# Optimization experiments

Measured on AMD Instinct MI355X. Metric: run time of the kernel, lower is better.

## Reference

```python
import math
import jax, jax.numpy as jnp
import numpy as np

C1, D, NUM_HEADS, K_CH = 150, 32, 4, 10
GLOBAL_TOPK_RATIO = 0.08


def _pos2d(h, w, dim):
    d2 = dim // 2
    div = jnp.exp(jnp.arange(0, d2, 2, dtype=jnp.float32) * (-(math.log(10000.0) / d2)))
    def axis_pe(n):
        ang = jnp.arange(n, dtype=jnp.float32)[:, None] * div[None, :]
        pe = jnp.zeros((n, d2), dtype=jnp.float32)
        pe = pe.at[:, 0::2].set(jnp.sin(ang))
        pe = pe.at[:, 1::2].set(jnp.cos(ang))
        return pe
    pe_y = axis_pe(h)  # [h, d2]
    pe_x = axis_pe(w)  # [w, d2]
    return jnp.concatenate([
        jnp.broadcast_to(pe_y[:, None, :], (h, w, d2)),
        jnp.broadcast_to(pe_x[None, :, :], (h, w, d2)),
    ], axis=-1)  # [h, w, dim]


def setup_inputs() -> dict:
    key = jax.random.key(0)
    ks = jax.random.split(key, 7)
    B = 1024
    return {
        "x": jax.random.uniform(ks[0], (B, 1, 28, 28), dtype=jnp.float32),
        "conv1_w": jax.random.normal(ks[1], (C1, 1, 9, 9), dtype=jnp.float32) * 0.05,
        "channel_embed": jax.random.normal(ks[2], (C1, D), dtype=jnp.float32) * 0.02,
        "in_proj_w": jax.random.normal(ks[3], (3 * D, D), dtype=jnp.float32) * (1.0 / math.sqrt(D)),
        "in_proj_b": jnp.zeros((3 * D,), dtype=jnp.float32),
        "out_proj_w": jax.random.normal(ks[4], (D, D), dtype=jnp.float32) * (1.0 / math.sqrt(D)),
        "out_proj_b": jnp.zeros((D,), dtype=jnp.float32),
    }


def reference(x, conv1_w, channel_embed, in_proj_w, in_proj_b, out_proj_w, out_proj_b):
    # conv1 + relu: [B,1,28,28] -> [B,150,14,14]
    A = jax.nn.relu(jax.lax.conv_general_dilated(
        x, conv1_w, window_strides=(2, 2), padding=((4, 4), (4, 4)),
        dimension_numbers=("NCHW", "OIHW", "NCHW")))
    B, C, H, W = A.shape
    total = C * H * W
    k_global = max(1, int(math.ceil(GLOBAL_TOPK_RATIO * total)))
    A_flat = A.reshape(B, -1)
    # global kthvalue threshold: k_global-th largest per sample
    thresh = jax.lax.top_k(A_flat, k_global)[0][:, -1:]
    A_global = (A_flat * (A_flat >= thresh)).reshape(B, C, H, W)
    # per-location channel top-k + scatter
    v = jnp.transpose(A_global, (0, 2, 3, 1))  # [B,H,W,C]
    topv, topi = jax.lax.top_k(v, K_CH)        # [B,H,W,k]
    N = B * H * W
    logits = jnp.zeros((N, C), v.dtype).at[
        jnp.arange(N)[:, None], topi.reshape(N, K_CH)
    ].set(topv.reshape(N, K_CH)).reshape(v.shape)
    # normalize by per-sample global max (guard zero)
    flat_logits = logits.reshape(B, -1)
    gmax = jnp.max(flat_logits, axis=1, keepdims=True)
    normed = jnp.where(gmax == 0, 0.0, flat_logits / jnp.where(gmax == 0, 1.0, gmax))
    sparse_weights = normed.reshape(logits.shape)  # [B,H,W,C]
    # channel embedding + 2D sinusoidal PE
    loc_emb = jnp.einsum("bhwc,cd->bhwd", sparse_weights, channel_embed)
    loc_emb = loc_emb + _pos2d(H, W, D)[None]
    seq = loc_emb.reshape(B, H * W, D)
    # 1-layer MHA (self-attention, batch_first)
    qkv = seq @ in_proj_w.T + in_proj_b  # [B,S,3D]
    q, k, vv = jnp.split(qkv, 3, axis=-1)
    hd = D // NUM_HEADS
    def heads(t):
        return jnp.transpose(t.reshape(B, H * W, NUM_HEADS, hd), (0, 2, 1, 3))
    q, k, vv = heads(q), heads(k), heads(vv)
    attn = jax.nn.softmax(jnp.einsum("bnsd,bntd->bnst", q, k) / math.sqrt(hd), axis=-1)
    ctx = jnp.einsum("bnst,bntd->bnsd", attn, vv)
    ctx = jnp.transpose(ctx, (0, 2, 1, 3)).reshape(B, H * W, D)
    attn_out = ctx @ out_proj_w.T + out_proj_b  # [B, 196, 32]
    return attn_out
```

## Files before the change

kernel.cpp:

```cpp
#include <hip/hip_runtime.h>
#include <math.h>

#define NC1 150
#define HW 196
#define NB 1024
#define DD 32
#define NHD 4
#define HDIM 8
#define KG 2352
#define KCH 10
#define CAP 48
#define CVS 49
#define CES 36

#define UNI_F 17552
#define XT_OFF 0
#define WT_OFF 8232
#define CV_OFF 0
#define CC_OFF 9604
#define CNT_OFF 11956
#define CE_OFF 12152

__global__ void pos2d_kernel(float* __restrict__ pos) {
  int i = blockIdx.x * 256 + threadIdx.x;
  if (i >= HW * DD) return;
  int s = i >> 5, d = i & 31;
  int h = s / 14, w = s % 14;
  int p = (d < 16) ? h : w;
  int dd = (d < 16) ? d : d - 16;
  int j = dd >> 1;
  float dv = expf(-(logf(10000.0f) / 16.0f) * (float)(2 * j));
  float ang = (float)p * dv;
  pos[i] = (dd & 1) ? cosf(ang) : sinf(ang);
}

__global__ void prep_kernel(const float* __restrict__ cw, float* __restrict__ wtg) {
  int i = blockIdx.x * 256 + threadIdx.x;
  if (i >= 84 * 152) return;
  int k = i / 152, c = i - k * 152;
  wtg[i] = (k < 81 && c < NC1) ? cw[c * 81 + k] : 0.f;
}

__global__ __launch_bounds__(1024, 8) void fused_kernel(const float* __restrict__ x,
                                                        const float* __restrict__ wtg,
                                                        const float* __restrict__ CE,
                                                        const float* __restrict__ pos,
                                                        float* __restrict__ seqo) {
  __shared__ alignas(16) float uni[UNI_F];
  __shared__ alignas(16) float xs[784];
  __shared__ unsigned hist[2048];
  __shared__ unsigned wsum[4];
  __shared__ unsigned s_prefix, s_krem, s_max;

  int b = blockIdx.x, tid = threadIdx.x;
  int lane = tid & 63, wid = tid >> 6;

  if (tid < 196) ((float4*)xs)[tid] = ((const float4*)(x + (size_t)b * 784))[tid];
  if (tid == 0) { s_prefix = 0u; s_krem = KG; s_max = 0u; }
  __syncthreads();

  int cg = tid / 49;
  int g  = tid - cg * 49;
  bool act = (tid < 931);
  float acc[4][8];
#pragma unroll
  for (int i = 0; i < 4; ++i)
#pragma unroll
    for (int j = 0; j < 8; ++j) acc[i][j] = 0.f;

  float* XT = uni + XT_OFF;
  float* WT = uni + WT_OFF;

  for (int kb = 0; kb < 84; kb += 42) {
    for (int i = tid; i < 42 * 196; i += 1024) {
      int kk = i / 196, s = i - kk * 196;
      int k = kb + kk;
      float v = 0.f;
      if (k < 81) {
        int ki = k / 9, kj = k - ki * 9;
        int h = s / 14, w = s - h * 14;
        int r = 2 * h - 4 + ki, c = 2 * w - 4 + kj;
        if (r >= 0 && r < 28 && c >= 0 && c < 28) v = xs[r * 28 + c];
      }
      XT[i] = v;
    }
    for (int i = tid; i < (42 * 152) / 4; i += 1024)
      ((float4*)WT)[i] = ((const float4*)(wtg + kb * 152))[i];
    __syncthreads();
    if (act) {
      const float* xtp = XT + 4 * g;
      const float* wtp = WT + 8 * cg;
#pragma unroll 7
      for (int kk = 0; kk < 42; ++kk) {
        float4 xv = *(const float4*)(xtp + kk * 196);
        float4 w0 = *(const float4*)(wtp + kk * 152);
        float4 w1 = *(const float4*)(wtp + kk * 152 + 4);
        float xa[4] = {xv.x, xv.y, xv.z, xv.w};
        float wa[8] = {w0.x, w0.y, w0.z, w0.w, w1.x, w1.y, w1.z, w1.w};
#pragma unroll
        for (int i = 0; i < 4; ++i)
#pragma unroll
          for (int j = 0; j < 8; ++j) acc[i][j] += xa[i] * wa[j];
      }
    }
    __syncthreads();
  }

#pragma unroll
  for (int i = 0; i < 4; ++i)
#pragma unroll
    for (int j = 0; j < 8; ++j) acc[i][j] = fmaxf(acc[i][j], 0.f);

  for (int pass = 0; pass < 3; ++pass) {
    hist[tid] = 0u; hist[tid + 1024] = 0u;
    __syncthreads();
    int shift = (pass == 0) ? 21 : (pass == 1 ? 10 : 0);
    int bits = (pass == 2) ? 10 : 11;
    unsigned mask = (1u << bits) - 1u;
    unsigned pfx = s_prefix;
    unsigned krem = s_krem;
    int hishift = shift + bits;
    if (pass == 0) {
      unsigned mymax = 0u;
#pragma unroll
      for (int i = 0; i < 4; ++i)
#pragma unroll
        for (int j = 0; j < 8; ++j) {
          unsigned u = __float_as_uint(acc[i][j]);
          mymax = max(mymax, u);
          if (u) atomicAdd(&hist[u >> 21], 1u);
        }
#pragma unroll
      for (int st = 32; st >= 1; st >>= 1)
        mymax = max(mymax, (unsigned)__shfl_xor((int)mymax, st));
      if (lane == 0) atomicMax(&s_max, mymax);
    } else {
#pragma unroll
      for (int i = 0; i < 4; ++i)
#pragma unroll
        for (int j = 0; j < 8; ++j) {
          unsigned u = __float_as_uint(acc[i][j]);
          if (u && (u >> hishift) == pfx) atomicAdd(&hist[(u >> shift) & mask], 1u);
        }
    }
    __syncthreads();
    int segsz = (1 << bits) >> 8;
    unsigned segv = 0u, sufv = 0u;
    if (tid < 256) {
      for (int j = 0; j < segsz; ++j) segv += hist[tid * segsz + j];
      sufv = segv;
#pragma unroll
      for (int st = 1; st < 64; st <<= 1) {
        unsigned o = (unsigned)__shfl_down((int)sufv, st);
        if (lane + st < 64) sufv += o;
      }
      if (lane == 0) wsum[wid] = sufv;
    }
    __syncthreads();
    if (tid < 256) {
      unsigned tail = 0u;
      for (int ww = wid + 1; ww < 4; ++ww) tail += wsum[ww];
      sufv += tail;
      unsigned above = sufv - segv;
      if (above < krem && sufv >= krem) {
        unsigned cum = above;
        int dsel = tid * segsz;
        for (int d2 = segsz - 1; d2 >= 0; --d2) {
          int dd = tid * segsz + d2;
          if (cum + hist[dd] >= krem) { dsel = dd; break; }
          cum += hist[dd];
        }
        s_prefix = (pfx << bits) | (unsigned)dsel;
        s_krem = krem - cum;
      }
    }
    __syncthreads();
  }

  float* candV = uni + CV_OFF;
  unsigned char* candC = (unsigned char*)(uni + CC_OFF);
  unsigned* cnt = (unsigned*)(uni + CNT_OFF);
  if (tid < 196) cnt[tid] = 0u;
  __syncthreads();
  float T = __uint_as_float(s_prefix);
  if (act) {
#pragma unroll
    for (int i = 0; i < 4; ++i) {
      int loc = 4 * g + i;
#pragma unroll
      for (int j = 0; j < 8; ++j) {
        float v = acc[i][j];
        if (v >= T && v > 0.f) {
          unsigned slot = atomicAdd(&cnt[loc], 1u);
          if (slot < CAP) {
            candV[loc * CVS + slot] = v;
            candC[loc * CAP + slot] = (unsigned char)(8 * cg + j);
          }
        }
      }
    }
  }
  __syncthreads();

  float* CEs = uni + CE_OFF;
  if (tid >= 196) {
    for (int i = tid - 196; i < NC1 * 32; i += 1024 - 196) {
      int c = i >> 5, e = i & 31;
      CEs[c * CES + e] = CE[i];
    }
  }
  float tv[KCH]; int tc[KCH];
  if (tid < 196) {
    int loc = tid;
    unsigned n = cnt[loc]; if (n > CAP) n = CAP;
#pragma unroll
    for (int k = 0; k < KCH; ++k) { tv[k] = 0.f; tc[k] = 0; }
    for (unsigned jj = 0; jj < n; ++jj) {
      float v = candV[loc * CVS + jj];
      int c = candC[loc * CAP + jj];
      if (v > tv[KCH - 1] || (v == tv[KCH - 1] && c < tc[KCH - 1])) {
        float iv = v; int ic = c;
#pragma unroll
        for (int j = 0; j < KCH; ++j) {
          bool gt = (iv > tv[j]) || (iv == tv[j] && ic < tc[j]);
          float nv = gt ? iv : tv[j]; int nc = gt ? ic : tc[j];
          float ov = gt ? tv[j] : iv; int oc = gt ? tc[j] : ic;
          tv[j] = nv; tc[j] = nc; iv = ov; ic = oc;
        }
      }
    }
  }
  __syncthreads();

  if (tid < 196) {
    float gm = __uint_as_float(s_max);
    float gi = (gm == 0.0f) ? 0.0f : 1.0f / gm;
    float acc2[32];
#pragma unroll
    for (int e = 0; e < 32; ++e) acc2[e] = 0.f;
#pragma unroll
    for (int k = 0; k < KCH; ++k) {
      float v = tv[k];
      const float4* cr = (const float4*)(CEs + tc[k] * CES);
#pragma unroll
      for (int e4 = 0; e4 < 8; ++e4) {
        float4 cv = cr[e4];
        acc2[e4 * 4 + 0] += v * cv.x;
        acc2[e4 * 4 + 1] += v * cv.y;
        acc2[e4 * 4 + 2] += v * cv.z;
        acc2[e4 * 4 + 3] += v * cv.w;
      }
    }
    float* op = seqo + ((size_t)b * HW + tid) * DD;
    const float* pr = pos + tid * DD;
#pragma unroll
    for (int e4 = 0; e4 < 8; ++e4) {
      float4 pv = ((const float4*)pr)[e4];
      float4 o;
      o.x = acc2[e4 * 4 + 0] * gi + pv.x;
      o.y = acc2[e4 * 4 + 1] * gi + pv.y;
      o.z = acc2[e4 * 4 + 2] * gi + pv.z;
      o.w = acc2[e4 * 4 + 3] * gi + pv.w;
      ((float4*)op)[e4] = o;
    }
  }
}

__global__ __launch_bounds__(256) void attn_kernel(const float* __restrict__ seq,
                                                   const float* __restrict__ Wqkv,
                                                   const float* __restrict__ bqkv,
                                                   float* __restrict__ ctxo) {
  __shared__ float sq[HW * HDIM], sk[HW * HDIM], sv[HW * HDIM];
  __shared__ float swq[24 * DD];
  __shared__ float sbq[24];
  __shared__ unsigned s_kk;
  int blk = blockIdx.x;
  int b = blk >> 2, h = blk & 3;
  int tid = threadIdx.x;
  for (int i = tid; i < 24 * DD; i += 256) {
    int r = i >> 5, e = i & 31;
    int grow = (r >> 3) * DD + h * HDIM + (r & 7);
    swq[i] = Wqkv[grow * DD + e];
  }
  if (tid < 24) sbq[tid] = bqkv[(tid >> 3) * DD + h * HDIM + (tid & 7)];
  if (tid == 0) s_kk = 0u;
  __syncthreads();
  if (tid < HW) {
    int s = tid;
    const float* row = seq + ((size_t)b * HW + s) * DD;
    float xr[32];
#pragma unroll
    for (int e = 0; e < 8; ++e) {
      float4 f = ((const float4*)row)[e];
      xr[e * 4 + 0] = f.x; xr[e * 4 + 1] = f.y; xr[e * 4 + 2] = f.z; xr[e * 4 + 3] = f.w;
    }
    float kk = 0.f;
#pragma unroll
    for (int r = 0; r < 24; ++r) {
      const float* wr = swq + r * DD;
      float acc = sbq[r];
#pragma unroll
      for (int e = 0; e < DD; e += 4) {
        float4 wv = *(const float4*)(wr + e);
        acc += xr[e + 0] * wv.x + xr[e + 1] * wv.y + xr[e + 2] * wv.z + xr[e + 3] * wv.w;
      }
      int which = r >> 3, d = r & 7;
      if (which == 0) sq[s * HDIM + d] = acc;
      else if (which == 1) { sk[s * HDIM + d] = acc; kk += acc * acc; }
      else sv[s * HDIM + d] = acc;
    }
    atomicMax(&s_kk, __float_as_uint(kk));
  }
  __syncthreads();
  if (tid >= HW) return;
  int qr = tid;
  float qreg[HDIM];
  float qq = 0.f;
#pragma unroll
  for (int d = 0; d < HDIM; ++d) { qreg[d] = sq[qr * HDIM + d]; qq += qreg[d] * qreg[d]; }
  const float scale = 0.3535533905932738f;
  float kkmax = __uint_as_float(s_kk);
  float negM = -sqrtf(qq * kkmax) * scale;
  float l = 0.f, ctx[HDIM];
#pragma unroll
  for (int d = 0; d < HDIM; ++d) ctx[d] = 0.f;
#pragma unroll 2
  for (int t = 0; t < HW; ++t) {
    const float* kr = sk + t * HDIM;
    float sc = 0.f;
#pragma unroll
    for (int d = 0; d < HDIM; ++d) sc += qreg[d] * kr[d];
    float p = __expf(fmaf(sc, scale, negM));
    l += p;
    const float* vr = sv + t * HDIM;
#pragma unroll
    for (int d = 0; d < HDIM; ++d) ctx[d] += p * vr[d];
  }
  float inv = 1.0f / l;
  float* op = ctxo + ((size_t)b * HW + qr) * DD + h * HDIM;
  float4 o0, o1;
  o0.x = ctx[0] * inv; o0.y = ctx[1] * inv; o0.z = ctx[2] * inv; o0.w = ctx[3] * inv;
  o1.x = ctx[4] * inv; o1.y = ctx[5] * inv; o1.z = ctx[6] * inv; o1.w = ctx[7] * inv;
  ((float4*)op)[0] = o0; ((float4*)op)[1] = o1;
}

__global__ __launch_bounds__(256) void outproj_kernel(const float* __restrict__ ctx,
                                                      const float* __restrict__ Wo,
                                                      const float* __restrict__ bo,
                                                      float* __restrict__ out) {
  __shared__ float sw[32 * 32];
  __shared__ float sb2[32];
  int tid = threadIdx.x;
  for (int i = tid; i < 1024; i += 256) sw[i] = Wo[i];
  if (tid < 32) sb2[tid] = bo[tid];
  __syncthreads();
  size_t row = (size_t)blockIdx.x * 256 + tid;
  const float* cr = ctx + row * 32;
  float xr[32];
#pragma unroll
  for (int e = 0; e < 8; ++e) {
    float4 f = ((const float4*)cr)[e];
    xr[e * 4 + 0] = f.x; xr[e * 4 + 1] = f.y; xr[e * 4 + 2] = f.z; xr[e * 4 + 3] = f.w;
  }
  float* op = out + row * 32;
#pragma unroll
  for (int d4 = 0; d4 < 8; ++d4) {
    float4 o;
    float* oo = (float*)&o;
#pragma unroll
    for (int q = 0; q < 4; ++q) {
      int d = d4 * 4 + q;
      float acc = sb2[d];
      const float* wr = sw + d * 32;
#pragma unroll
      for (int e = 0; e < 32; e += 4) {
        float4 wv = *(const float4*)(wr + e);
        acc += xr[e + 0] * wv.x + xr[e + 1] * wv.y + xr[e + 2] * wv.z + xr[e + 3] * wv.w;
      }
      oo[q] = acc;
    }
    ((float4*)op)[d4] = o;
  }
}

extern "C" void kernel_launch(void* const* d_in, const int* in_sizes, int n_in,
                              void* d_out, int out_size, void* d_ws, size_t ws_size,
                              hipStream_t stream) {
  const float* x  = (const float*)d_in[0];
  const float* cw = (const float*)d_in[1];
  const float* ce = (const float*)d_in[2];
  const float* wq = (const float*)d_in[3];
  const float* bq = (const float*)d_in[4];
  const float* wo = (const float*)d_in[5];
  const float* bo = (const float*)d_in[6];
  float* out = (float*)d_out;
  float* ws  = (float*)d_ws;

  float* ctx = ws;
  float* pos = ws + (size_t)NB * HW * DD;
  float* wtg = pos + HW * DD;

  prep_kernel<<<(84 * 152 + 255) / 256, 256, 0, stream>>>(cw, wtg);
  pos2d_kernel<<<(HW * DD + 255) / 256, 256, 0, stream>>>(pos);
  fused_kernel<<<NB, 1024, 0, stream>>>(x, wtg, ce, pos, out);
  attn_kernel<<<NB * NHD, 256, 0, stream>>>(out, wq, bq, ctx);
  outproj_kernel<<<(NB * HW * DD) / (256 * 32), 256, 0, stream>>>(ctx, wo, bo, out);
}
```

Measured before the change: 422.5 us.

## Process all heads of a sample in one attention block with interleaved K/V

Restructures the attention kernel so that one 832-thread block handles all four heads of a sample instead of one 256-thread block per head. In the old layout 60 of 256 threads sat idle; now only 48 of 832 do. The seq row is still loaded once per thread, and each thread computes only its own head's Q, K and V. K and V are interleaved in 16-float rows of shared memory so the inner loop can use float4 loads, and Q stays in registers. This trades higher shared-memory use per block and fewer blocks for better thread utilisation and vectorised LDS access.

```diff
diff --git a/kernel.cpp b/kernel.cpp
--- a/kernel.cpp
+++ b/kernel.cpp
@@ -266,27 +266,28 @@
   }
 }
 
-__global__ __launch_bounds__(256) void attn_kernel(const float* __restrict__ seq,
-                                                   const float* __restrict__ Wqkv,
-                                                   const float* __restrict__ bqkv,
-                                                   float* __restrict__ ctxo) {
-  __shared__ float sq[HW * HDIM], sk[HW * HDIM], sv[HW * HDIM];
-  __shared__ float swq[24 * DD];
-  __shared__ float sbq[24];
-  __shared__ unsigned s_kk;
-  int blk = blockIdx.x;
-  int b = blk >> 2, h = blk & 3;
-  int tid = threadIdx.x;
-  for (int i = tid; i < 24 * DD; i += 256) {
-    int r = i >> 5, e = i & 31;
-    int grow = (r >> 3) * DD + h * HDIM + (r & 7);
-    swq[i] = Wqkv[grow * DD + e];
-  }
-  if (tid < 24) sbq[tid] = bqkv[(tid >> 3) * DD + h * HDIM + (tid & 7)];
-  if (tid == 0) s_kk = 0u;
-  __syncthreads();
-  if (tid < HW) {
-    int s = tid;
+__global__ __launch_bounds__(832, 7) void attn_kernel(const float* __restrict__ seq,
+                                                      const float* __restrict__ Wqkv,
+                                                      const float* __restrict__ bqkv,
+                                                      float* __restrict__ ctxo) {
+  __shared__ alignas(16) float kvs[NHD * HW * 16];
+  __shared__ alignas(16) float swq[96 * DD];
+  __shared__ float sbq[96];
+  __shared__ unsigned s_kk[NHD];
+
+  int b = blockIdx.x, tid = threadIdx.x;
+  for (int i = tid; i < (96 * DD) / 4; i += 832)
+    ((float4*)swq)[i] = ((const float4*)Wqkv)[i];
+  if (tid < 96) sbq[tid] = bqkv[tid];
+  if (tid < NHD) s_kk[tid] = 0u;
+
+  int h = tid / HW;
+  int s = tid - h * HW;
+  bool act = (tid < NHD * HW);
+  __syncthreads();
+
+  float q[8]; float qq = 0.f;
+  if (act) {
     const float* row = seq + ((size_t)b * HW + s) * DD;
     float xr[32];
 #pragma unroll
@@ -294,53 +295,80 @@
       float4 f = ((const float4*)row)[e];
       xr[e * 4 + 0] = f.x; xr[e * 4 + 1] = f.y; xr[e * 4 + 2] = f.z; xr[e * 4 + 3] = f.w;
     }
-    float kk = 0.f;
-#pragma unroll
-    for (int r = 0; r < 24; ++r) {
-      const float* wr = swq + r * DD;
-      float acc = sbq[r];
+    float* kvrow = kvs + ((size_t)h * HW + s) * 16;
+    {
+      float ka[8]; float kk = 0.f;
+#pragma unroll
+      for (int d = 0; d < 8; ++d) {
+        const float* wr = swq + (32 + h * HDIM + d) * DD;
+        float acc = sbq[32 + h * HDIM + d];
+#pragma unroll
+        for (int e = 0; e < DD; e += 4) {
+          float4 wv = *(const float4*)(wr + e);
+          acc += xr[e + 0] * wv.x + xr[e + 1] * wv.y + xr[e + 2] * wv.z + xr[e + 3] * wv.w;
+        }
+        ka[d] = acc; kk += acc * acc;
+      }
+      float4 k0 = {ka[0], ka[1], ka[2], ka[3]}, k1 = {ka[4], ka[5], ka[6], ka[7]};
+      ((float4*)kvrow)[0] = k0; ((float4*)kvrow)[1] = k1;
+      atomicMax(&s_kk[h], __float_as_uint(kk));
+    }
+    {
+      float va[8];
+#pragma unroll
+      for (int d = 0; d < 8; ++d) {
+        const float* wr = swq + (64 + h * HDIM + d) * DD;
+        float acc = sbq[64 + h * HDIM + d];
+#pragma unroll
+        for (int e = 0; e < DD; e += 4) {
+          float4 wv = *(const float4*)(wr + e);
+          acc += xr[e + 0] * wv.x + xr[e + 1] * wv.y + xr[e + 2] * wv.z + xr[e + 3] * wv.w;
+        }
+        va[d] = acc;
+      }
+      float4 v0 = {va[0], va[1], va[2], va[3]}, v1 = {va[4], va[5], va[6], va[7]};
+      ((float4*)kvrow)[2] = v0; ((float4*)kvrow)[3] = v1;
+    }
+#pragma unroll
+    for (int d = 0; d < 8; ++d) {
+      const float* wr = swq + (h * HDIM + d) * DD;
+      float acc = sbq[h * HDIM + d];
 #pragma unroll
       for (int e = 0; e < DD; e += 4) {
         float4 wv = *(const float4*)(wr + e);
         acc += xr[e + 0] * wv.x + xr[e + 1] * wv.y + xr[e + 2] * wv.z + xr[e + 3] * wv.w;
       }
-      int which = r >> 3, d = r & 7;
-      if (which == 0) sq[s * HDIM + d] = acc;
-      else if (which == 1) { sk[s * HDIM + d] = acc; kk += acc * acc; }
-      else sv[s * HDIM + d] = acc;
-    }
-    atomicMax(&s_kk, __float_as_uint(kk));
-  }
-  __syncthreads();
-  if (tid >= HW) return;
-  int qr = tid;
-  float qreg[HDIM];
-  float qq = 0.f;
-#pragma unroll
-  for (int d = 0; d < HDIM; ++d) { qreg[d] = sq[qr * HDIM + d]; qq += qreg[d] * qreg[d]; }
+      q[d] = acc; qq += acc * acc;
+    }
+  }
+  __syncthreads();
+  if (!act) return;
+
   const float scale = 0.3535533905932738f;
-  float kkmax = __uint_as_float(s_kk);
+  float kkmax = __uint_as_float(s_kk[h]);
   float negM = -sqrtf(qq * kkmax) * scale;
-  float l = 0.f, ctx[HDIM];
-#pragma unroll
-  for (int d = 0; d < HDIM; ++d) ctx[d] = 0.f;
-#pragma unroll 2
+  float l = 0.f;
+  float c0 = 0.f, c1 = 0.f, c2 = 0.f, c3 = 0.f, c4 = 0.f, c5 = 0.f, c6 = 0.f, c7 = 0.f;
+  const float4* kp = (const float4*)(kvs + (size_t)h * HW * 16);
+#pragma unroll 4
   for (int t = 0; t < HW; ++t) {
-    const float* kr = sk + t * HDIM;
-    float sc = 0.f;
-#pragma unroll
-    for (int d = 0; d < HDIM; ++d) sc += qreg[d] * kr[d];
+    float4 k0 = kp[0], k1 = kp[1], v0 = kp[2], v1 = kp[3];
+    kp += 4;
+    float sc = q[0] * k0.x;
+    sc = fmaf(q[1], k0.y, sc); sc = fmaf(q[2], k0.z, sc); sc = fmaf(q[3], k0.w, sc);
+    sc = fmaf(q[4], k1.x, sc); sc = fmaf(q[5], k1.y, sc); sc = fmaf(q[6], k1.z, sc);
+    sc = fmaf(q[7], k1.w, sc);
     float p = __expf(fmaf(sc, scale, negM));
     l += p;
-    const float* vr = sv + t * HDIM;
-#pragma unroll
-    for (int d = 0; d < HDIM; ++d) ctx[d] += p * vr[d];
+    c0 = fmaf(p, v0.x, c0); c1 = fmaf(p, v0.y, c1); c2 = fmaf(p, v0.z, c2);
+    c3 = fmaf(p, v0.w, c3); c4 = fmaf(p, v1.x, c4); c5 = fmaf(p, v1.y, c5);
+    c6 = fmaf(p, v1.z, c6); c7 = fmaf(p, v1.w, c7);
   }
   float inv = 1.0f / l;
-  float* op = ctxo + ((size_t)b * HW + qr) * DD + h * HDIM;
+  float* op = ctxo + ((size_t)b * HW + s) * DD + h * HDIM;
   float4 o0, o1;
-  o0.x = ctx[0] * inv; o0.y = ctx[1] * inv; o0.z = ctx[2] * inv; o0.w = ctx[3] * inv;
-  o1.x = ctx[4] * inv; o1.y = ctx[5] * inv; o1.z = ctx[6] * inv; o1.w = ctx[7] * inv;
+  o0.x = c0 * inv; o0.y = c1 * inv; o0.z = c2 * inv; o0.w = c3 * inv;
+  o1.x = c4 * inv; o1.y = c5 * inv; o1.z = c6 * inv; o1.w = c7 * inv;
   ((float4*)op)[0] = o0; ((float4*)op)[1] = o1;
 }
 
@@ -403,6 +431,6 @@
   prep_kernel<<<(84 * 152 + 255) / 256, 256, 0, stream>>>(cw, wtg);
   pos2d_kernel<<<(HW * DD + 255) / 256, 256, 0, stream>>>(pos);
   fused_kernel<<<NB, 1024, 0, stream>>>(x, wtg, ce, pos, out);
-  attn_kernel<<<NB * NHD, 256, 0, stream>>>(out, wq, bq, ctx);
+  attn_kernel<<<NB, 832, 0, stream>>>(out, wq, bq, ctx);
   outproj_kernel<<<(NB * HW * DD) / (256 * 32), 256, 0, stream>>>(ctx, wo, bo, out);
 }
```

New measurement: 571.5 us. +35.3%, slower.
